# Optimization experiments

Measured on AMD Instinct MI355X. Metric: run time of the kernel, lower is better.

Reference implementation:

```python
import jax, jax.numpy as jnp
import numpy as np

B, L, D = 2, 2048, 1024
H = 16
C = 128            # chunk_size
N = L // C         # num chunks
SCALE = float(np.sqrt(D))  # softmax_scale = sqrt(d_model)


def setup_inputs() -> dict:
    key = jax.random.key(0)
    ks = jax.random.split(key, 5)
    return {
        "x": jax.random.normal(ks[0], (B, L, D), dtype=jnp.float32),
        "w_qkv": jax.random.normal(ks[1], (D, 3 * D), dtype=jnp.float32) * (1.0 / np.sqrt(D)),
        "b_qkv": jax.random.normal(ks[2], (3 * D,), dtype=jnp.float32) * 0.02,
        "w_o": jax.random.normal(ks[3], (D, D), dtype=jnp.float32) * (1.0 / np.sqrt(D)),
        "b_o": jax.random.normal(ks[4], (D,), dtype=jnp.float32) * 0.02,
    }


def reference(x, w_qkv, b_qkv, w_o, b_o):
    b, l, d = x.shape
    hd = d // H
    qkv = x @ w_qkv + b_qkv                         # (B,L,3D)
    q, k, v = jnp.split(qkv, 3, axis=-1)
    q = q.reshape(b, l, H, hd)
    k = k.reshape(b, l, H, hd)
    v = v.reshape(b, l, H, hd)

    q_chunks = q.reshape(b, N, C, H, hd)
    k_chunks = k.reshape(b, N, C, H, hd)
    # mean_pool over the chunk dim
    q_pool = q_chunks.mean(axis=2)                  # (B,N,H,hd)
    k_pool = k_chunks.mean(axis=2)

    token2chunk = jnp.einsum('blhd,bnhd->bhln', q, k_pool)          # (B,H,L,N)
    chunk2token = jnp.einsum('bnhd,bnchd->bhnc', q_pool, k_chunks)  # (B,H,N,C)
    # outer product over (n,c) -> full (B,H,L,L) score matrix
    A = token2chunk[..., :, None] * chunk2token[:, :, None, :, :]   # (B,H,L,N,C)
    A = A.reshape(b, H, l, l)

    # direct intra-chunk attention overwrites the diagonal blocks
    direct = jnp.einsum('bnqhd,bnkhd->bhnqk', q_chunks, k_chunks)   # (B,H,N,C,C)
    A6 = A.reshape(b, H, N, C, N, C)
    eye = jnp.eye(N, dtype=bool)[:, None, :, None]                  # (N,1,N,1)
    A6 = jnp.where(eye, direct[:, :, :, :, None, :], A6)
    A = A6.reshape(b, H, l, l)

    # causal mask applied multiplicatively (masked scores become 0, NOT -inf)
    causal = jnp.tril(jnp.ones((l, l), dtype=bool))
    A = jnp.where(causal, A, 0.0) / SCALE
    A = jax.nn.softmax(A, axis=-1)

    out = jnp.einsum('bhqv,bvhd->bhqd', A, v)       # (B,H,L,hd)
    out = out.transpose(0, 2, 1, 3).reshape(b, l, d)
    return out @ w_o + b_o
```

## Files before the change

kernel.cpp:

```cpp
#include <hip/hip_runtime.h>
#include <math.h>

#define B_   2
#define L_   2048
#define D_   1024
#define H_   16
#define HD_  64
#define C_   128
#define N_   16
#define INV_SCALE 0.03125f

typedef _Float16 h8 __attribute__((ext_vector_type(8)));
typedef _Float16 h4 __attribute__((ext_vector_type(4)));
typedef float    f4 __attribute__((ext_vector_type(4)));

#define MFMA16(a, b, c) __builtin_amdgcn_mfma_f32_16x16x32_f16((a), (b), (c), 0, 0, 0)

__device__ __forceinline__ void gl_lds16(const void* g, void* l) {
  __builtin_amdgcn_global_load_lds(
      (const __attribute__((address_space(1))) void*)g,
      (__attribute__((address_space(3))) void*)l, 16, 0, 0);
}

#define SBAR()  do { __builtin_amdgcn_sched_barrier(0); \
                     __builtin_amdgcn_s_barrier();      \
                     __builtin_amdgcn_sched_barrier(0); } while (0)
#define LGKM0() do { asm volatile("s_waitcnt lgkmcnt(0)" ::: "memory"); \
                     __builtin_amdgcn_sched_barrier(0); } while (0)
#define VMW(n)  do { asm volatile("s_waitcnt vmcnt(" #n ")" ::: "memory"); \
                     __builtin_amdgcn_sched_barrier(0); } while (0)

__global__ __launch_bounds__(256) void prep_kernel(
    const float* __restrict__ X, _Float16* __restrict__ Xh,
    const float* __restrict__ Wq, _Float16* __restrict__ WqT,
    const float* __restrict__ Wo, _Float16* __restrict__ WoT)
{
  __shared__ float ts[32][36];
  const int tid = threadIdx.x;
  const int id = blockIdx.x;
  if (id < 4096) {
    int i = id * 1024 + tid * 4;
    float4 v = *(const float4*)(X + i);
    h4 o = { (_Float16)v.x, (_Float16)v.y, (_Float16)v.z, (_Float16)v.w };
    *(h4*)(Xh + i) = o;
    return;
  }
  const float* W; _Float16* WT; int Nc, bx, by;
  if (id < 7168) {
    int idx = id - 4096;
    W = Wq; WT = WqT; Nc = 3072; bx = idx % 96; by = idx / 96;
  } else {
    int idx = id - 7168;
    W = Wo; WT = WoT; Nc = 1024; bx = idx & 31; by = idx >> 5;
  }
  const int n0 = bx * 32, k0 = by * 32;
  {
    int kr = tid >> 3, nc4 = (tid & 7) * 4;
    float4 v = *(const float4*)&W[(size_t)(k0 + kr) * Nc + n0 + nc4];
    ts[kr][nc4+0] = v.x; ts[kr][nc4+1] = v.y; ts[kr][nc4+2] = v.z; ts[kr][nc4+3] = v.w;
  }
  __syncthreads();
  {
    int nr = tid >> 3, kc4 = (tid & 7) * 4;
    h4 o = { (_Float16)ts[kc4+0][nr], (_Float16)ts[kc4+1][nr],
             (_Float16)ts[kc4+2][nr], (_Float16)ts[kc4+3][nr] };
    *(h4*)&WT[(size_t)(n0 + nr) * 1024 + k0 + kc4] = o;
  }
}

__global__ __launch_bounds__(512, 2) void qkv256_kernel(
    const _Float16* __restrict__ A, const _Float16* __restrict__ Bt,
    const float* __restrict__ bias,
    _Float16* __restrict__ Qh, _Float16* __restrict__ Kh, _Float16* __restrict__ VT,
    float* __restrict__ QP, float* __restrict__ KP, float* __restrict__ VCS)
{
  __shared__ __align__(16) _Float16 As[2][16384];
  __shared__ __align__(16) _Float16 Bs[2][12288];

  const int tid = threadIdx.x;
  const int w = tid >> 6, lane = tid & 63;
  const int q = lane >> 4, r = lane & 15, r7 = r & 7;
  const int wm = w >> 2, wn = w & 3;

  const int id = blockIdx.x, xcd = id & 7, slot = id >> 3;
  const int m0 = ((xcd >> 1) * 4 + (slot & 3)) * 256;
  const int n0 = ((xcd & 1) * 8 + (slot >> 2)) * 192;

  const int srow = tid >> 3;
  const int spart = (tid & 7) ^ (srow & 7);
  const _Float16* Asrc = A  + (size_t)(m0 + srow) * 1024 + spart * 8;
  const _Float16* Bsrc = Bt + (size_t)(n0 + srow) * 1024 + spart * 8;
  const int ldst = w * 512;

  const int aoffb = (wm * 128 + r) * 64;
  const int boffb = (wn * 48 + r) * 64;
  const int k0s = (q ^ r7) << 3;
  const int k1s = ((4 + q) ^ r7) << 3;

  auto stA = [&](int cc, int ko, int qq) {
    gl_lds16(Asrc + (size_t)qq * 65536 + ko, &As[cc][qq * 4096 + ldst]);
  };
  auto stB = [&](int cc, int ko, int qq) {
    gl_lds16(Bsrc + (size_t)qq * 65536 + ko, &Bs[cc][qq * 4096 + ldst]);
  };

  f4 acc[8][3];
  #pragma unroll
  for (int m = 0; m < 8; ++m)
    #pragma unroll
    for (int n = 0; n < 3; ++n) acc[m][n] = (f4){0.f, 0.f, 0.f, 0.f};

  stB(0, 0, 0); stB(0, 0, 1); stB(0, 0, 2);
  stA(0, 0, 0); stA(0, 0, 2); stA(0, 0, 1); stA(0, 0, 3);
  VMW(2);
  SBAR();

  for (int t = 0; t < 16; ++t) {
    const int c = t & 1;
    const _Float16* __restrict__ Ab = As[c];
    const _Float16* __restrict__ Bb = Bs[c];
    const int kt = (t + 1) << 6;
    const bool pf = (t < 15);
    h8 af[4], bf[3];

    #pragma unroll
    for (int m = 0; m < 4; ++m) af[m] = *(const h8*)&Ab[aoffb + m * 1024 + k0s];
    #pragma unroll
    for (int n = 0; n < 3; ++n) bf[n] = *(const h8*)&Bb[boffb + n * 1024 + k0s];
    if (pf) { stB(c ^ 1, kt, 0); stB(c ^ 1, kt, 1); }
    SBAR();
    LGKM0();
    __builtin_amdgcn_s_setprio(1);
    #pragma unroll
    for (int m = 0; m < 4; ++m)
      #pragma unroll
      for (int n = 0; n < 3; ++n) acc[m][n] = MFMA16(af[m], bf[n], acc[m][n]);
    __builtin_amdgcn_s_setprio(0);
    __builtin_amdgcn_sched_barrier(0);
    if (pf) { VMW(2); } else { VMW(0); }
    SBAR();

    #pragma unroll
    for (int m = 0; m < 4; ++m) af[m] = *(const h8*)&Ab[aoffb + (4 + m) * 1024 + k0s];
    if (pf) { stB(c ^ 1, kt, 2); stA(c ^ 1, kt, 0); }
    SBAR();
    LGKM0();
    __builtin_amdgcn_s_setprio(1);
    #pragma unroll
    for (int m = 0; m < 4; ++m)
      #pragma unroll
      for (int n = 0; n < 3; ++n) acc[4 + m][n] = MFMA16(af[m], bf[n], acc[4 + m][n]);
    __builtin_amdgcn_s_setprio(0);
    __builtin_amdgcn_sched_barrier(0);
    SBAR();

    #pragma unroll
    for (int m = 0; m < 4; ++m) af[m] = *(const h8*)&Ab[aoffb + m * 1024 + k1s];
    #pragma unroll
    for (int n = 0; n < 3; ++n) bf[n] = *(const h8*)&Bb[boffb + n * 1024 + k1s];
    if (pf) { stA(c ^ 1, kt, 2); stA(c ^ 1, kt, 1); }
    SBAR();
    LGKM0();
    __builtin_amdgcn_s_setprio(1);
    #pragma unroll
    for (int m = 0; m < 4; ++m)
      #pragma unroll
      for (int n = 0; n < 3; ++n) acc[m][n] = MFMA16(af[m], bf[n], acc[m][n]);
    __builtin_amdgcn_s_setprio(0);
    __builtin_amdgcn_sched_barrier(0);
    SBAR();

    #pragma unroll
    for (int m = 0; m < 4; ++m) af[m] = *(const h8*)&Ab[aoffb + (4 + m) * 1024 + k1s];
    if (pf) {
      stA(c ^ 1, kt, 3);
      VMW(2);
    }
    SBAR();
    LGKM0();
    __builtin_amdgcn_s_setprio(1);
    #pragma unroll
    for (int m = 0; m < 4; ++m)
      #pragma unroll
      for (int n = 0; n < 3; ++n) acc[4 + m][n] = MFMA16(af[m], bf[n], acc[4 + m][n]);
    __builtin_amdgcn_s_setprio(0);
    __builtin_amdgcn_sched_barrier(0);
    SBAR();
  }

  const int rb = m0 + wm * 128;
  const int b2 = rb >> 11;
  const int nch = (rb & 2047) >> 7;
  #pragma unroll
  for (int tc = 0; tc < 3; ++tc) {
    const int gn = n0 + wn * 48 + tc * 16 + r;
    const float bj = bias[gn];
    const int which = gn >> 10, rem = gn & 1023;
    const int h2 = rem >> 6, d2 = rem & 63;
    if (which < 2) {
      _Float16* dst = which == 0 ? Qh : Kh;
      #pragma unroll
      for (int m = 0; m < 8; ++m)
        #pragma unroll
        for (int i = 0; i < 4; ++i) {
          const int gm = rb + m * 16 + q * 4 + i;
          const int l2 = gm & 2047;
          dst[(((size_t)(b2 * H_ + h2)) * L_ + l2) * HD_ + d2] =
              (_Float16)(acc[m][tc][i] + bj);
        }
    } else {
      #pragma unroll
      for (int m = 0; m < 8; ++m) {
        const int gm0 = rb + m * 16 + q * 4;
        const int l2 = gm0 & 2047;
        h4 hv = { (_Float16)(acc[m][tc][0] + bj), (_Float16)(acc[m][tc][1] + bj),
                  (_Float16)(acc[m][tc][2] + bj), (_Float16)(acc[m][tc][3] + bj) };
        *(h4*)&VT[((size_t)(b2 * H_ + h2) * HD_ + d2) * L_ + l2] = hv;
      }
    }
    float s2 = 0.f;
    #pragma unroll
    for (int m = 0; m < 8; ++m)
      #pragma unroll
      for (int i = 0; i < 4; ++i) s2 += acc[m][tc][i];
    s2 += __shfl_xor(s2, 16);
    s2 += __shfl_xor(s2, 32);
    if (q == 0) {
      const size_t o = (((size_t)(b2 * H_ + h2)) * N_ + nch) * HD_ + d2;
      if (which == 0)      QP[o] = s2 * (1.f / 128.f) + bj;
      else if (which == 1) KP[o] = s2 * (1.f / 128.f) + bj;
      else                 VCS[o] = s2 + 128.f * bj;
    }
  }
}

template<int MT>
__global__ __launch_bounds__(256, 4) void gemm16_kernel(
    const _Float16* __restrict__ A, const _Float16* __restrict__ Bt,
    const float* __restrict__ bias,
    _Float16* __restrict__ Qh, _Float16* __restrict__ Kh, _Float16* __restrict__ VT,
    float* __restrict__ out,
    float* __restrict__ QP, float* __restrict__ KP, float* __restrict__ VCS,
    int Kd, int mode)
{
  constexpr int SM = MT / 32;
  __shared__ __align__(16) _Float16 As[2][MT * 32];
  __shared__ __align__(16) _Float16 Bs[2][4096];
  __shared__ float cred[2][128];
  const int tid = threadIdx.x;
  const int lane = tid & 63, w = tid >> 6;
  const int q = lane >> 4, r = lane & 15;
  const int mb = (w >> 1) * (MT / 2);
  const int nb = (w & 1) * 64;

  int m0, n0;
  {
    const int id = blockIdx.x;
    const int xcd = id & 7, slot = id >> 3;
    if constexpr (MT == 128) {
      n0 = (xcd * 3 + (slot % 3)) * 128;
      m0 = (slot / 3) * 128;
    } else {
      m0 = (xcd * 8 + (slot >> 3)) * 64;
      n0 = (slot & 7) * 128;
    }
  }

  const int Rr = tid >> 2;
  const int cd = (tid & 3) ^ ((Rr >> 1) & 3);
  const _Float16* Ag = A + (size_t)(m0 + Rr) * Kd + cd * 8;
  const _Float16* Bg = Bt + (size_t)(n0 + Rr) * Kd + cd * 8;
  const size_t rowStep = (size_t)64 * Kd;

  f4 acc[SM][4];
  #pragma unroll
  for (int s = 0; s < SM; ++s)
    #pragma unroll
    for (int t = 0; t < 4; ++t) acc[s][t] = (f4){0.f, 0.f, 0.f, 0.f};

  const int nIter = Kd >> 5;
  const int koff = (q ^ ((r >> 1) & 3)) << 3;

  auto stage = [&](int bf, int kt) {
    _Float16* Asl = &As[bf][w * 512];
    _Float16* Bsl = &Bs[bf][w * 512];
    gl_lds16(Ag + kt, Asl);
    if constexpr (MT == 128) gl_lds16(Ag + kt + rowStep, Asl + 2048);
    gl_lds16(Bg + kt, Bsl);
    gl_lds16(Bg + kt + rowStep, Bsl + 2048);
  };

  stage(0, 0);

  for (int it = 0; it < nIter; ++it) {
    __syncthreads();
    if (it + 1 < nIter) stage((it + 1) & 1, (it + 1) << 5);
    const _Float16* Ab = As[it & 1];
    const _Float16* Bb = Bs[it & 1];
    h8 af[SM], bf4[4];
    #pragma unroll
    for (int s = 0; s < SM; ++s)
      af[s] = *(const h8*)&Ab[(mb + s * 16 + r) * 32 + koff];
    #pragma unroll
    for (int t = 0; t < 4; ++t)
      bf4[t] = *(const h8*)&Bb[(nb + t * 16 + r) * 32 + koff];
    #pragma unroll
    for (int s = 0; s < SM; ++s)
      #pragma unroll
      for (int t = 0; t < 4; ++t)
        acc[s][t] = MFMA16(af[s], bf4[t], acc[s][t]);
  }

  if (mode == 0) {
    #pragma unroll
    for (int t = 0; t < 4; ++t) {
      int gn = n0 + nb + t * 16 + r;
      float bj = bias[gn];
      int which = gn >> 10, rem = gn & 1023;
      int h2 = rem >> 6, d2 = rem & 63;
      if (which < 2) {
        _Float16* dst = which == 0 ? Qh : Kh;
        #pragma unroll
        for (int s = 0; s < SM; ++s)
          #pragma unroll
          for (int i = 0; i < 4; ++i) {
            int gm = m0 + mb + s * 16 + q * 4 + i;
            int b2 = gm >> 11, l2 = gm & 2047;
            dst[(((size_t)(b2 * H_ + h2)) * L_ + l2) * HD_ + d2] =
                (_Float16)(acc[s][t][i] + bj);
          }
      } else {
        #pragma unroll
        for (int s = 0; s < SM; ++s) {
          int gm0 = m0 + mb + s * 16 + q * 4;
          int b2 = gm0 >> 11, l2 = gm0 & 2047;
          h4 hv = { (_Float16)(acc[s][t][0] + bj), (_Float16)(acc[s][t][1] + bj),
                    (_Float16)(acc[s][t][2] + bj), (_Float16)(acc[s][t][3] + bj) };
          *(h4*)&VT[((size_t)(b2 * H_ + h2) * HD_ + d2) * L_ + l2] = hv;
        }
      }
    }
    float colsum[4];
    #pragma unroll
    for (int t = 0; t < 4; ++t) {
      float s2 = 0.f;
      #pragma unroll
      for (int s = 0; s < SM; ++s)
        #pragma unroll
        for (int i = 0; i < 4; ++i) s2 += acc[s][t][i];
      s2 += __shfl_xor(s2, 16);
      s2 += __shfl_xor(s2, 32);
      colsum[t] = s2;
    }
    if (q == 0) {
      #pragma unroll
      for (int t = 0; t < 4; ++t)
        cred[w >> 1][nb + t * 16 + r] = colsum[t];
    }
    __syncthreads();
    if (tid < 128) {
      int jj = tid;
      float ssum = cred[0][jj] + cred[1][jj];
      int gn = n0 + jj;
      float bj = bias[gn];
      int which = gn >> 10, rem = gn & 1023;
      int h2 = rem >> 6, d2 = rem & 63;
      int b2 = m0 >> 11, nch = (m0 & 2047) >> 7;
      size_t o = (((size_t)(b2 * H_ + h2)) * N_ + nch) * HD_ + d2;
      if (which == 0)      QP[o] = ssum * (1.f / 128.f) + bj;
      else if (which == 1) KP[o] = ssum * (1.f / 128.f) + bj;
      else                 VCS[o] = ssum + 128.f * bj;
    }
  } else {
    #pragma unroll
    for (int t = 0; t < 4; ++t) {
      int gn = n0 + nb + t * 16 + r;
      float bj = bias[gn];
      #pragma unroll
      for (int s = 0; s < SM; ++s)
        #pragma unroll
        for (int i = 0; i < 4; ++i) {
          int gm = m0 + mb + s * 16 + q * 4 + i;
          out[(size_t)gm * 1024 + gn] = acc[s][t][i] + bj;
        }
    }
  }
}

__global__ __launch_bounds__(128) void pool2_kernel(
    const float* __restrict__ QP, const _Float16* __restrict__ Kh,
    const float* __restrict__ VCS,
    float* __restrict__ C2T, float* __restrict__ C2TMX, float* __restrict__ C2TMN,
    float* __restrict__ CSUF)
{
  __shared__ float qp_s[64];
  __shared__ float red[4];
  if (blockIdx.x >= 512) {
    int bh = blockIdx.x - 512, d = threadIdx.x;
    if (d < 64) {
      float run = 0.f;
      for (int n = N_ - 1; n >= 0; --n) {
        size_t o = ((size_t)bh * N_ + n) * HD_ + d;
        CSUF[o] = run;
        run += VCS[o];
      }
    }
    return;
  }
  int bh = blockIdx.x >> 4, n = blockIdx.x & 15, tid = threadIdx.x;
  int w = tid >> 6, lane = tid & 63;
  if (tid < 64) qp_s[tid] = QP[((size_t)bh * N_ + n) * HD_ + tid];
  const _Float16* kr = Kh + (((size_t)bh * L_) + n * C_ + tid) * HD_;
  h8 kv[8];
  #pragma unroll
  for (int c8 = 0; c8 < 8; ++c8) kv[c8] = *(const h8*)(kr + c8 * 8);
  __syncthreads();
  float s = 0.f;
  #pragma unroll
  for (int c8 = 0; c8 < 8; ++c8)
    #pragma unroll
    for (int j = 0; j < 8; ++j)
      s = fmaf((float)kv[c8][j], qp_s[c8 * 8 + j], s);
  C2T[((size_t)bh * N_ + n) * C_ + tid] = s;
  float mx = s, mn = s;
  #pragma unroll
  for (int st = 1; st <= 32; st <<= 1) {
    mx = fmaxf(mx, __shfl_xor(mx, st));
    mn = fminf(mn, __shfl_xor(mn, st));
  }
  if (lane == 0) { red[w * 2] = mx; red[w * 2 + 1] = mn; }
  __syncthreads();
  if (tid == 0) {
    C2TMX[bh * N_ + n] = fmaxf(red[0], red[2]);
    C2TMN[bh * N_ + n] = fminf(red[1], red[3]);
  }
}

__global__ __launch_bounds__(512, 4) void attn4_kernel(
    const _Float16* __restrict__ Qh, const _Float16* __restrict__ Kh,
    const _Float16* __restrict__ VT,
    const float* __restrict__ C2T, const float* __restrict__ C2TMX,
    const float* __restrict__ C2TMN, const float* __restrict__ CSUF,
    const float* __restrict__ KP, _Float16* __restrict__ AOh)
{
  __shared__ __align__(16) _Float16 buf0[8192];
  __shared__ __align__(16) _Float16 buf1[8192];
  __shared__ __align__(16) _Float16 buf2[8192];
  __shared__ __align__(16) _Float16 kp_s[1024];
  __shared__ __align__(16) float c2t_s[2][128];

  const int tid = threadIdx.x;
  const int w = tid >> 6, lane = tid & 63;
  const int q = lane >> 4, r = lane & 15;
  const int r7 = r & 7;
  const int id = blockIdx.x;
  const int bh = ((id & 7) << 2) + ((id >> 3) & 3);
  const int nq = 15 - (id >> 5);
  const int l0 = nq * 128;
  const int rowA = l0 + w * 16 + r;
  const int pcw = w * 16 + r;
  const size_t bhL = (size_t)bh * L_;
  const int b2 = bh >> 4, h2 = bh & 15;

  auto stageV = [&](_Float16* buf, int n) {
    #pragma unroll
    for (int j2 = 0; j2 < 2; ++j2) {
      int f = j2 * 512 + tid;
      int d = f >> 4, p = f & 15;
      int c16 = p ^ (d & 7);
      gl_lds16(VT + ((size_t)bh * HD_ + d) * L_ + n * C_ + c16 * 8,
               buf + (size_t)(j2 * 512 + w * 64) * 8);
    }
  };
  auto stageK = [&](_Float16* buf, int n) {
    #pragma unroll
    for (int j2 = 0; j2 < 2; ++j2) {
      int f = j2 * 512 + tid;
      int c = f >> 3, p = f & 7;
      int ck = p ^ (c & 7);
      gl_lds16(Kh + (bhL + n * C_ + c) * HD_ + ck * 8,
               buf + (size_t)(j2 * 512 + w * 64) * 8);
    }
  };
  auto stageC = [&](int bf, int n) {
    if (tid < 32)
      gl_lds16(C2T + ((size_t)bh * N_ + n) * C_ + tid * 4, &c2t_s[bf][0]);
  };

  if (tid < 256) {
    int n4 = tid >> 4, d4 = (tid & 15) * 4;
    float4 kpv = *(const float4*)&KP[((size_t)bh * N_ + n4) * HD_ + d4];
    int sd = ((((d4 >> 3) ^ (n4 & 7)) << 3) | (d4 & 7));
    h4 hv = { (_Float16)kpv.x, (_Float16)kpv.y, (_Float16)kpv.z, (_Float16)kpv.w };
    *(h4*)&kp_s[n4 * 64 + sd] = hv;
  }
  h8 qa0 = *(const h8*)(Qh + (bhL + rowA) * HD_ + q * 8);
  h8 qa1 = *(const h8*)(Qh + (bhL + rowA) * HD_ + 32 + q * 8);
  float mxL = C2TMX[bh * N_ + r];
  float mnL = C2TMN[bh * N_ + r];
  stageK(buf0, nq);
  stageV(buf2, nq);
  if (nq >= 1) stageC(0, nq - 1);
  __syncthreads();

  f4 tvacc = (f4){0.f, 0.f, 0.f, 0.f};
  {
    h8 kpa0 = *(const h8*)&kp_s[r * 64 + ((q ^ r7) << 3)];
    h8 kpa1 = *(const h8*)&kp_s[r * 64 + (((4 + q) ^ r7) << 3)];
    tvacc = MFMA16(kpa0, qa0, tvacc);
    tvacc = MFMA16(kpa1, qa1, tvacc);
  }
  float tvs[4];
  #pragma unroll
  for (int i = 0; i < 4; ++i) tvs[i] = tvacc[i] * INV_SCALE;

  float pm = -1e30f;
  #pragma unroll
  for (int i = 0; i < 4; ++i) {
    int n = q * 4 + i;
    float mx = __shfl(mxL, n);
    float mn = __shfl(mnL, n);
    float cm = fmaxf(tvs[i] * mx, tvs[i] * mn);
    pm = (n < nq) ? fmaxf(pm, cm) : pm;
  }
  pm = fmaxf(pm, __shfl_xor(pm, 16));
  pm = fmaxf(pm, __shfl_xor(pm, 32));

  f4 sc[8];
  #pragma unroll
  for (int u = 0; u < 8; ++u) sc[u] = (f4){0.f, 0.f, 0.f, 0.f};
  #pragma unroll
  for (int u = 0; u < 8; ++u) {
    h8 kb0 = *(const h8*)&buf0[(u * 16 + r) * 64 + ((q ^ r7) << 3)];
    h8 kb1 = *(const h8*)&buf0[(u * 16 + r) * 64 + (((4 + q) ^ r7) << 3)];
    sc[u] = MFMA16(qa0, kb0, sc[u]);
    sc[u] = MFMA16(qa1, kb1, sc[u]);
  }

  float rm[4] = {-1e30f, -1e30f, -1e30f, -1e30f};
  #pragma unroll
  for (int u = 0; u < 8; ++u) {
    int lcol = u * 16 + r;
    #pragma unroll
    for (int i = 0; i < 4; ++i) {
      int lrow = w * 16 + q * 4 + i;
      float v = sc[u][i] * INV_SCALE;
      v = (lcol <= lrow) ? v : -1e30f;
      sc[u][i] = v;
      rm[i] = fmaxf(rm[i], v);
    }
  }
  #pragma unroll
  for (int i = 0; i < 4; ++i) {
    rm[i] = fmaxf(rm[i], __shfl_xor(rm[i], 1));
    rm[i] = fmaxf(rm[i], __shfl_xor(rm[i], 2));
    rm[i] = fmaxf(rm[i], __shfl_xor(rm[i], 4));
    rm[i] = fmaxf(rm[i], __shfl_xor(rm[i], 8));
  }
  const int srcl = (r >> 2) << 4;
  const int ri = r & 3;
  float t0 = __shfl(rm[0], srcl), t1 = __shfl(rm[1], srcl);
  float t2 = __shfl(rm[2], srcl), t3 = __shfl(rm[3], srcl);
  float myrm = ri == 0 ? t0 : ri == 1 ? t1 : ri == 2 ? t2 : t3;

  const float M = fmaxf(fmaxf(pm, myrm), 0.f);
  const float e0 = __expf(-M);
  float Mc[4];
  #pragma unroll
  for (int i = 0; i < 4; ++i) Mc[i] = __shfl(M, (q << 2) + i);

  float cs[4] = {0.f, 0.f, 0.f, 0.f};
  #pragma unroll
  for (int u = 0; u < 8; ++u)
    #pragma unroll
    for (int i = 0; i < 4; ++i) {
      float v = sc[u][i];
      float p = (v > -1e29f) ? __expf(v - Mc[i]) : 0.f;
      sc[u][i] = p;
      cs[i] += p;
    }
  #pragma unroll
  for (int i = 0; i < 4; ++i) {
    cs[i] += __shfl_xor(cs[i], 1);
    cs[i] += __shfl_xor(cs[i], 2);
    cs[i] += __shfl_xor(cs[i], 4);
    cs[i] += __shfl_xor(cs[i], 8);
  }
  float c0 = __shfl(cs[0], srcl), c1 = __shfl(cs[1], srcl);
  float c2 = __shfl(cs[2], srcl), c3 = __shfl(cs[3], srcl);
  float den = ri == 0 ? c0 : ri == 1 ? c1 : ri == 2 ? c2 : c3;

  __syncthreads();

  _Float16* pw = (w < 4) ? (buf0 + w * 2048) : (buf1 + (w - 4) * 2048);
  #pragma unroll
  for (int u = 0; u < 8; ++u)
    #pragma unroll
    for (int i = 0; i < 4; ++i) {
      int row = q * 4 + i, col = u * 16 + r;
      pw[row * 128 + ((((col >> 3) ^ (row & 7)) << 3) | (col & 7))] =
          (_Float16)sc[u][i];
    }

  f4 oacc[4], sacc[4];
  #pragma unroll
  for (int t = 0; t < 4; ++t) {
    oacc[t] = (f4){0.f, 0.f, 0.f, 0.f};
    sacc[t] = (f4){0.f, 0.f, 0.f, 0.f};
  }
  #pragma unroll
  for (int s = 0; s < 4; ++s) {
    h8 pa = *(const h8*)&pw[r * 128 + (((s * 4 + q) ^ r7) << 3)];
    h8 mk;
    #pragma unroll
    for (int j2 = 0; j2 < 8; ++j2)
      mk[j2] = (_Float16)((s * 32 + q * 8 + j2 > pcw) ? 1.f : 0.f);
    #pragma unroll
    for (int t = 0; t < 4; ++t) {
      h8 vb = *(const h8*)&buf2[(t * 16 + r) * 128 + (((s * 4 + q) ^ r7) << 3)];
      oacc[t] = MFMA16(pa, vb, oacc[t]);
      sacc[t] = MFMA16(mk, vb, sacc[t]);
    }
  }

  __syncthreads();
  if (nq >= 1) stageV(buf1, nq - 1);

  for (int n = nq - 1; n >= 0; --n) {
    const int k = nq - 1 - n;
    _Float16* curb = (k & 1) ? buf2 : buf1;
    __syncthreads();
    if (n >= 1) {
      stageV((k & 1) ? buf1 : buf2, n - 1);
      stageC((k + 1) & 1, n - 1);
    }
    int i0 = n & 3;
    float tvx = i0 == 0 ? tvs[0] : i0 == 1 ? tvs[1] : i0 == 2 ? tvs[2] : tvs[3];
    float tvn = __shfl(tvx, ((n >> 2) << 4) + r);
    float csum = 0.f;
    const float* c2p = c2t_s[k & 1];
    #pragma unroll
    for (int s = 0; s < 4; ++s) {
      const float* cp = &c2p[s * 32 + q * 8];
      float4 ca = *(const float4*)cp;
      float4 cb = *(const float4*)(cp + 4);
      float p0 = __expf(tvn * ca.x - M), p1 = __expf(tvn * ca.y - M);
      float p2 = __expf(tvn * ca.z - M), p3 = __expf(tvn * ca.w - M);
      float p4 = __expf(tvn * cb.x - M), p5 = __expf(tvn * cb.y - M);
      float p6 = __expf(tvn * cb.z - M), p7 = __expf(tvn * cb.w - M);
      csum += p0 + p1 + p2 + p3 + p4 + p5 + p6 + p7;
      h8 pa = { (_Float16)p0, (_Float16)p1, (_Float16)p2, (_Float16)p3,
                (_Float16)p4, (_Float16)p5, (_Float16)p6, (_Float16)p7 };
      #pragma unroll
      for (int t = 0; t < 4; ++t) {
        h8 vb = *(const h8*)&curb[(t * 16 + r) * 128 + (((s * 4 + q) ^ r7) << 3)];
        oacc[t] = MFMA16(pa, vb, oacc[t]);
      }
    }
    csum += __shfl_xor(csum, 16);
    csum += __shfl_xor(csum, 32);
    den += csum;
  }

  int cnt = (L_ - 1) - rowA;
  den += e0 * (float)cnt;
  float e0r[4], dnr[4];
  #pragma unroll
  for (int i = 0; i < 4; ++i) {
    e0r[i] = __shfl(e0,  (q << 2) + i);
    dnr[i] = __shfl(den, (q << 2) + i);
  }
  #pragma unroll
  for (int t = 0; t < 4; ++t) {
    int d = t * 16 + r;
    float csf = CSUF[((size_t)bh * N_ + nq) * HD_ + d];
    #pragma unroll
    for (int i = 0; i < 4; ++i) {
      int row = l0 + w * 16 + q * 4 + i;
      float suffix = sacc[t][i] + csf;
      float o = (oacc[t][i] + e0r[i] * suffix) / dnr[i];
      AOh[((size_t)b2 * L_ + row) * D_ + h2 * HD_ + d] = (_Float16)o;
    }
  }
}

extern "C" void kernel_launch(void* const* d_in, const int* in_sizes, int n_in,
                              void* d_out, int out_size, void* d_ws, size_t ws_size,
                              hipStream_t stream)
{
  (void)in_sizes; (void)n_in; (void)out_size; (void)ws_size;
  const float* x     = (const float*)d_in[0];
  const float* w_qkv = (const float*)d_in[1];
  const float* b_qkv = (const float*)d_in[2];
  const float* w_o   = (const float*)d_in[3];
  const float* b_o   = (const float*)d_in[4];
  float* out = (float*)d_out;

  char* p = (char*)d_ws;
  _Float16* xh   = (_Float16*)p; p += (size_t)4194304 * 2;
  _Float16* wqT  = (_Float16*)p; p += (size_t)3145728 * 2;
  _Float16* woT  = (_Float16*)p; p += (size_t)1048576 * 2;
  _Float16* Qh   = (_Float16*)p; p += (size_t)4194304 * 2;
  _Float16* Kh   = (_Float16*)p; p += (size_t)4194304 * 2;
  _Float16* VT   = (_Float16*)p; p += (size_t)4194304 * 2;
  _Float16* AOh  = (_Float16*)p; p += (size_t)4194304 * 2;
  float*    C2T  = (float*)p;    p += (size_t)65536 * 4;
  float*    QP   = (float*)p;    p += (size_t)32768 * 4;
  float*    KP   = (float*)p;    p += (size_t)32768 * 4;
  float*    VCS  = (float*)p;    p += (size_t)32768 * 4;
  float*    CSUF = (float*)p;    p += (size_t)32768 * 4;
  float*    MXa  = (float*)p;    p += (size_t)512 * 4;
  float*    MNa  = (float*)p;    p += (size_t)512 * 4;

  prep_kernel<<<8192, 256, 0, stream>>>(x, xh, w_qkv, wqT, w_o, woT);
  qkv256_kernel<<<256, 512, 0, stream>>>(
      xh, wqT, b_qkv, Qh, Kh, VT, QP, KP, VCS);
  pool2_kernel<<<544, 128, 0, stream>>>(QP, Kh, VCS, C2T, MXa, MNa, CSUF);
  attn4_kernel<<<512, 512, 0, stream>>>(
      Qh, Kh, VT, C2T, MXa, MNa, CSUF, KP, AOh);
  gemm16_kernel<64><<<512, 256, 0, stream>>>(
      AOh, woT, b_o, nullptr, nullptr, nullptr, out, nullptr, nullptr, nullptr, D_, 1);
}
```

Baseline: 172.1 us.

## Transpose diagonal score MFMA, switch to exp2 with folded log2e scale, prefetch LDS operands

Folds log2(e) into the softmax scale so every exponential becomes a native exp2 with an fma instead of a subtract followed by expf. The diagonal-block score MFMA now uses swapped operands, so each lane holds one query row. That removes the 16-lane row-max and row-sum shuffle reductions and lets P be written to LDS as packed half4 stores. The PV and chunk-loop MFMAs get software-prefetched V/P/c2t LDS operands, and the loop's denominator reduction moves out of the loop. This raises register pressure and depends on the new swizzled store layout matching the reads.

```diff
diff --git a/kernel.cpp b/kernel.cpp
--- a/kernel.cpp
+++ b/kernel.cpp
@@ -9,12 +9,19 @@
 #define C_   128
 #define N_   16
 #define INV_SCALE 0.03125f
+#define SCL2 0.0450842200f
 
 typedef _Float16 h8 __attribute__((ext_vector_type(8)));
 typedef _Float16 h4 __attribute__((ext_vector_type(4)));
 typedef float    f4 __attribute__((ext_vector_type(4)));
 
 #define MFMA16(a, b, c) __builtin_amdgcn_mfma_f32_16x16x32_f16((a), (b), (c), 0, 0, 0)
+
+#if __has_builtin(__builtin_amdgcn_exp2f)
+#define EXP2(x) __builtin_amdgcn_exp2f(x)
+#else
+#define EXP2(x) exp2f(x)
+#endif
 
 __device__ __forceinline__ void gl_lds16(const void* g, void* l) {
   __builtin_amdgcn_global_load_lds(
@@ -512,7 +519,7 @@
   }
   float tvs[4];
   #pragma unroll
-  for (int i = 0; i < 4; ++i) tvs[i] = tvacc[i] * INV_SCALE;
+  for (int i = 0; i < 4; ++i) tvs[i] = tvacc[i] * SCL2;
 
   float pm = -1e30f;
   #pragma unroll
@@ -529,78 +536,59 @@
   f4 sc[8];
   #pragma unroll
   for (int u = 0; u < 8; ++u) sc[u] = (f4){0.f, 0.f, 0.f, 0.f};
+  {
+    h8 kc0 = *(const h8*)&buf0[r * 64 + ((q ^ r7) << 3)];
+    h8 kc1 = *(const h8*)&buf0[r * 64 + (((4 + q) ^ r7) << 3)];
+    #pragma unroll
+    for (int u = 0; u < 8; ++u) {
+      h8 kn0, kn1;
+      if (u < 7) {
+        kn0 = *(const h8*)&buf0[((u + 1) * 16 + r) * 64 + ((q ^ r7) << 3)];
+        kn1 = *(const h8*)&buf0[((u + 1) * 16 + r) * 64 + (((4 + q) ^ r7) << 3)];
+      }
+      sc[u] = MFMA16(kc0, qa0, sc[u]);
+      sc[u] = MFMA16(kc1, qa1, sc[u]);
+      kc0 = kn0; kc1 = kn1;
+    }
+  }
+
+  float rm = -1e30f;
+  #pragma unroll
+  for (int u = 0; u < 8; ++u)
+    #pragma unroll
+    for (int i = 0; i < 4; ++i) {
+      int lcol = u * 16 + q * 4 + i;
+      float v = sc[u][i] * SCL2;
+      v = (lcol <= pcw) ? v : -1e30f;
+      sc[u][i] = v;
+      rm = fmaxf(rm, v);
+    }
+  rm = fmaxf(rm, __shfl_xor(rm, 16));
+  rm = fmaxf(rm, __shfl_xor(rm, 32));
+
+  const float M = fmaxf(fmaxf(pm, rm), 0.f);
+  const float e0 = EXP2(-M);
+
+  __syncthreads();
+
+  _Float16* pw = (w < 4) ? (buf0 + w * 2048) : (buf1 + (w - 4) * 2048);
+  const int pwbase = r * 128 + ((q & 1) << 2);
+  float csl = 0.f;
   #pragma unroll
   for (int u = 0; u < 8; ++u) {
-    h8 kb0 = *(const h8*)&buf0[(u * 16 + r) * 64 + ((q ^ r7) << 3)];
-    h8 kb1 = *(const h8*)&buf0[(u * 16 + r) * 64 + (((4 + q) ^ r7) << 3)];
-    sc[u] = MFMA16(qa0, kb0, sc[u]);
-    sc[u] = MFMA16(qa1, kb1, sc[u]);
-  }
-
-  float rm[4] = {-1e30f, -1e30f, -1e30f, -1e30f};
-  #pragma unroll
-  for (int u = 0; u < 8; ++u) {
-    int lcol = u * 16 + r;
-    #pragma unroll
-    for (int i = 0; i < 4; ++i) {
-      int lrow = w * 16 + q * 4 + i;
-      float v = sc[u][i] * INV_SCALE;
-      v = (lcol <= lrow) ? v : -1e30f;
-      sc[u][i] = v;
-      rm[i] = fmaxf(rm[i], v);
-    }
-  }
-  #pragma unroll
-  for (int i = 0; i < 4; ++i) {
-    rm[i] = fmaxf(rm[i], __shfl_xor(rm[i], 1));
-    rm[i] = fmaxf(rm[i], __shfl_xor(rm[i], 2));
-    rm[i] = fmaxf(rm[i], __shfl_xor(rm[i], 4));
-    rm[i] = fmaxf(rm[i], __shfl_xor(rm[i], 8));
-  }
-  const int srcl = (r >> 2) << 4;
-  const int ri = r & 3;
-  float t0 = __shfl(rm[0], srcl), t1 = __shfl(rm[1], srcl);
-  float t2 = __shfl(rm[2], srcl), t3 = __shfl(rm[3], srcl);
-  float myrm = ri == 0 ? t0 : ri == 1 ? t1 : ri == 2 ? t2 : t3;
-
-  const float M = fmaxf(fmaxf(pm, myrm), 0.f);
-  const float e0 = __expf(-M);
-  float Mc[4];
-  #pragma unroll
-  for (int i = 0; i < 4; ++i) Mc[i] = __shfl(M, (q << 2) + i);
-
-  float cs[4] = {0.f, 0.f, 0.f, 0.f};
-  #pragma unroll
-  for (int u = 0; u < 8; ++u)
+    h4 pv4;
     #pragma unroll
     for (int i = 0; i < 4; ++i) {
       float v = sc[u][i];
-      float p = (v > -1e29f) ? __expf(v - Mc[i]) : 0.f;
-      sc[u][i] = p;
-      cs[i] += p;
-    }
-  #pragma unroll
-  for (int i = 0; i < 4; ++i) {
-    cs[i] += __shfl_xor(cs[i], 1);
-    cs[i] += __shfl_xor(cs[i], 2);
-    cs[i] += __shfl_xor(cs[i], 4);
-    cs[i] += __shfl_xor(cs[i], 8);
-  }
-  float c0 = __shfl(cs[0], srcl), c1 = __shfl(cs[1], srcl);
-  float c2 = __shfl(cs[2], srcl), c3 = __shfl(cs[3], srcl);
-  float den = ri == 0 ? c0 : ri == 1 ? c1 : ri == 2 ? c2 : c3;
-
-  __syncthreads();
-
-  _Float16* pw = (w < 4) ? (buf0 + w * 2048) : (buf1 + (w - 4) * 2048);
-  #pragma unroll
-  for (int u = 0; u < 8; ++u)
-    #pragma unroll
-    for (int i = 0; i < 4; ++i) {
-      int row = q * 4 + i, col = u * 16 + r;
-      pw[row * 128 + ((((col >> 3) ^ (row & 7)) << 3) | (col & 7))] =
-          (_Float16)sc[u][i];
-    }
+      float p = (v > -1e29f) ? EXP2(v - M) : 0.f;
+      csl += p;
+      pv4[i] = (_Float16)p;
+    }
+    *(h4*)&pw[pwbase + ((((u << 1) | (q >> 1)) ^ r7) << 3)] = pv4;
+  }
+  csl += __shfl_xor(csl, 16);
+  csl += __shfl_xor(csl, 32);
+  float den = csl;
 
   f4 oacc[4], sacc[4];
   #pragma unroll
@@ -608,27 +596,44 @@
     oacc[t] = (f4){0.f, 0.f, 0.f, 0.f};
     sacc[t] = (f4){0.f, 0.f, 0.f, 0.f};
   }
-  #pragma unroll
-  for (int s = 0; s < 4; ++s) {
-    h8 pa = *(const h8*)&pw[r * 128 + (((s * 4 + q) ^ r7) << 3)];
-    h8 mk;
-    #pragma unroll
-    for (int j2 = 0; j2 < 8; ++j2)
-      mk[j2] = (_Float16)((s * 32 + q * 8 + j2 > pcw) ? 1.f : 0.f);
-    #pragma unroll
-    for (int t = 0; t < 4; ++t) {
-      h8 vb = *(const h8*)&buf2[(t * 16 + r) * 128 + (((s * 4 + q) ^ r7) << 3)];
-      oacc[t] = MFMA16(pa, vb, oacc[t]);
-      sacc[t] = MFMA16(mk, vb, sacc[t]);
+  {
+    h8 pcur = *(const h8*)&pw[r * 128 + ((q ^ r7) << 3)];
+    h8 vcur[4];
+    #pragma unroll
+    for (int t = 0; t < 4; ++t)
+      vcur[t] = *(const h8*)&buf2[(t * 16 + r) * 128 + ((q ^ r7) << 3)];
+    #pragma unroll
+    for (int s = 0; s < 4; ++s) {
+      h8 pnxt; h8 vnxt[4];
+      if (s < 3) {
+        pnxt = *(const h8*)&pw[r * 128 + ((((s + 1) * 4 + q) ^ r7) << 3)];
+        #pragma unroll
+        for (int t = 0; t < 4; ++t)
+          vnxt[t] = *(const h8*)&buf2[(t * 16 + r) * 128 + ((((s + 1) * 4 + q) ^ r7) << 3)];
+      }
+      h8 mk;
+      #pragma unroll
+      for (int j2 = 0; j2 < 8; ++j2)
+        mk[j2] = (_Float16)((s * 32 + q * 8 + j2 > pcw) ? 1.f : 0.f);
+      #pragma unroll
+      for (int t = 0; t < 4; ++t) {
+        oacc[t] = MFMA16(pcur, vcur[t], oacc[t]);
+        sacc[t] = MFMA16(mk, vcur[t], sacc[t]);
+      }
+      pcur = pnxt;
+      #pragma unroll
+      for (int t = 0; t < 4; ++t) vcur[t] = vnxt[t];
     }
   }
 
   __syncthreads();
   if (nq >= 1) stageV(buf1, nq - 1);
 
+  float dsum = 0.f;
+  const float negM = -M;
   for (int n = nq - 1; n >= 0; --n) {
     const int k = nq - 1 - n;
-    _Float16* curb = (k & 1) ? buf2 : buf1;
+    const _Float16* curb = (k & 1) ? buf2 : buf1;
     __syncthreads();
     if (n >= 1) {
       stageV((k & 1) ? buf1 : buf2, n - 1);
@@ -637,30 +642,43 @@
     int i0 = n & 3;
     float tvx = i0 == 0 ? tvs[0] : i0 == 1 ? tvs[1] : i0 == 2 ? tvs[2] : tvs[3];
     float tvn = __shfl(tvx, ((n >> 2) << 4) + r);
-    float csum = 0.f;
     const float* c2p = c2t_s[k & 1];
+
+    f4 cca = *(const f4*)&c2p[q * 8];
+    f4 ccb = *(const f4*)&c2p[q * 8 + 4];
+    h8 vcur[4];
+    #pragma unroll
+    for (int t = 0; t < 4; ++t)
+      vcur[t] = *(const h8*)&curb[(t * 16 + r) * 128 + ((q ^ r7) << 3)];
+
     #pragma unroll
     for (int s = 0; s < 4; ++s) {
-      const float* cp = &c2p[s * 32 + q * 8];
-      float4 ca = *(const float4*)cp;
-      float4 cb = *(const float4*)(cp + 4);
-      float p0 = __expf(tvn * ca.x - M), p1 = __expf(tvn * ca.y - M);
-      float p2 = __expf(tvn * ca.z - M), p3 = __expf(tvn * ca.w - M);
-      float p4 = __expf(tvn * cb.x - M), p5 = __expf(tvn * cb.y - M);
-      float p6 = __expf(tvn * cb.z - M), p7 = __expf(tvn * cb.w - M);
-      csum += p0 + p1 + p2 + p3 + p4 + p5 + p6 + p7;
+      f4 can, cbn; h8 vnxt[4];
+      if (s < 3) {
+        can = *(const f4*)&c2p[(s + 1) * 32 + q * 8];
+        cbn = *(const f4*)&c2p[(s + 1) * 32 + q * 8 + 4];
+        #pragma unroll
+        for (int t = 0; t < 4; ++t)
+          vnxt[t] = *(const h8*)&curb[(t * 16 + r) * 128 + ((((s + 1) * 4 + q) ^ r7) << 3)];
+      }
+      float p0 = EXP2(fmaf(tvn, cca[0], negM)), p1 = EXP2(fmaf(tvn, cca[1], negM));
+      float p2 = EXP2(fmaf(tvn, cca[2], negM)), p3 = EXP2(fmaf(tvn, cca[3], negM));
+      float p4 = EXP2(fmaf(tvn, ccb[0], negM)), p5 = EXP2(fmaf(tvn, ccb[1], negM));
+      float p6 = EXP2(fmaf(tvn, ccb[2], negM)), p7 = EXP2(fmaf(tvn, ccb[3], negM));
+      dsum += p0 + p1 + p2 + p3 + p4 + p5 + p6 + p7;
       h8 pa = { (_Float16)p0, (_Float16)p1, (_Float16)p2, (_Float16)p3,
                 (_Float16)p4, (_Float16)p5, (_Float16)p6, (_Float16)p7 };
       #pragma unroll
-      for (int t = 0; t < 4; ++t) {
-        h8 vb = *(const h8*)&curb[(t * 16 + r) * 128 + (((s * 4 + q) ^ r7) << 3)];
-        oacc[t] = MFMA16(pa, vb, oacc[t]);
-      }
-    }
-    csum += __shfl_xor(csum, 16);
-    csum += __shfl_xor(csum, 32);
-    den += csum;
-  }
+      for (int t = 0; t < 4; ++t)
+        oacc[t] = MFMA16(pa, vcur[t], oacc[t]);
+      cca = can; ccb = cbn;
+      #pragma unroll
+      for (int t = 0; t < 4; ++t) vcur[t] = vnxt[t];
+    }
+  }
+  dsum += __shfl_xor(dsum, 16);
+  dsum += __shfl_xor(dsum, 32);
+  den += dsum;
 
   int cnt = (L_ - 1) - rowA;
   den += e0 * (float)cnt;
```

After: 171.4 us. About the same (-0.4%).
